# Optimization experiments

Hardware: AMD Instinct MI355X
Metric: run time of the kernel (lower is better)

The kernel has to match this reference:

```python
import jax, jax.numpy as jnp
import numpy as np

B, S, D = 64, 8192, 64

def setup_inputs() -> dict:
    key = jax.random.key(0)
    kq, kk, kv = jax.random.split(key, 3)
    q = jax.random.normal(kq, (B, S, D), dtype=jnp.float32)
    k = jax.random.normal(kk, (B, S, D), dtype=jnp.float32)
    v = jax.random.normal(kv, (B, S, D), dtype=jnp.float32)
    return {"q": q, "k": k, "v": v}

def _feature_map(x):
    # ELU(x) + 1
    return jax.nn.elu(x) + 1.0

def reference(q, k, v):
    qf = _feature_map(q)              # [B, S, D]
    kf = _feature_map(k)              # [B, S, D]
    k_sum = kf.sum(axis=-2)           # [B, D]
    kv = jnp.einsum('bsd,bse->bde', kf, v)        # [B, D, D]
    deno = jnp.maximum(jnp.einsum('bsd,bd->bs', qf, k_sum), 1e-4)  # [B, S]
    o = jnp.einsum('bsd,bde->bse', qf, kv) / deno[..., None]       # [B, S, D]
    return o
```

## Files before the change

kernel.cpp:

```cpp
#include <hip/hip_runtime.h>
#include <math.h>

#define BB 64
#define SS 8192
#define DD 64

constexpr int C1 = 8;
constexpr int CHUNK1 = SS / C1;
constexpr int TROWS  = 128;
constexpr int TILES1 = CHUNK1 / TROWS;

typedef __attribute__((ext_vector_type(8))) short bf16x8;
typedef __attribute__((ext_vector_type(4))) float f32x4;

__device__ __forceinline__ float fmap(float x) {
    return x > 0.0f ? x + 1.0f : __expf(x);
}

__device__ __forceinline__ short f2bf(float x) {
    unsigned int u = __float_as_uint(x);
    u += 0x7FFFu + ((u >> 16) & 1u);
    return (short)(u >> 16);
}

__device__ __forceinline__ void split8(const float* x, bf16x8& hi, bf16x8& lo) {
    #pragma unroll
    for (int i = 0; i < 8; ++i) {
        unsigned int u = __float_as_uint(x[i]);
        hi[i] = (short)(u >> 16);
        float l = x[i] - __uint_as_float(u & 0xFFFF0000u);
        lo[i] = f2bf(l);
    }
}

__device__ __forceinline__ void gload_lds16(const float* gsrc, float* ldst) {
    __builtin_amdgcn_global_load_lds(
        (const __attribute__((address_space(1))) unsigned int*)gsrc,
        (__attribute__((address_space(3))) unsigned int*)ldst,
        16, 0, 0);
}

__global__ __launch_bounds__(256) void phase1_kernel(
    const float* __restrict__ k,
    const float* __restrict__ v,
    float* __restrict__ kvT_ws,
    float* __restrict__ ksum_ws)
{
    __shared__ float Ks[2][TROWS * 64];
    __shared__ float Vs[2][TROWS * 64];

    const int t    = threadIdx.x;
    const int lane = t & 63;
    const int w    = t >> 6;
    const int g    = lane >> 4;
    const int c    = lane & 15;
    const int b    = blockIdx.y;

    const size_t base = (size_t)b * SS * DD + (size_t)blockIdx.x * CHUNK1 * DD;
    const float* kb = k + base;
    const float* vb = v + base;

    auto issue_tile = [&](int tt, int buf) {
        const float* kt = kb + tt * (TROWS * 64);
        const float* vt = vb + tt * (TROWS * 64);
        #pragma unroll
        for (int i = 0; i < 8; ++i) {
            const int Lidx = (w * 8 + i) * 64 + lane;
            const int s    = Lidx >> 4;
            const int p    = Lidx & 15;
            const int gch  = p ^ (((s >> 3) & 1) << 2);
            const int goff = s * 64 + gch * 4;
            const int loff = (w * 8 + i) * 256;
            gload_lds16(kt + goff, &Ks[buf][loff]);
            gload_lds16(vt + goff, &Vs[buf][loff]);
        }
    };

    f32x4 acc[4][4] = {};
    float ksa[4] = {};

    issue_tile(0, 0);
    __syncthreads();

    for (int tt = 0; tt < TILES1; ++tt) {
        const int cur = tt & 1;
        if (tt + 1 < TILES1) issue_tile(tt + 1, cur ^ 1);

        const float* Kc = Ks[cur];
        const float* Vc = Vs[cur];
        const int srow = w * 32 + g * 8;
        const int sw   = (g & 1) << 2;

        bf16x8 Ah[4], Al[4];
        #pragma unroll
        for (int et = 0; et < 4; ++et) {
            const int dc   = et * 16 + c;
            const int bidx = srow * 64 + ((((dc >> 2) ^ sw)) << 2) + (dc & 3);
            float x[8];
            #pragma unroll
            for (int i = 0; i < 8; ++i) x[i] = Vc[bidx + i * 64];
            split8(x, Ah[et], Al[et]);
        }
        #pragma unroll
        for (int dt = 0; dt < 4; ++dt) {
            const int dc   = dt * 16 + c;
            const int bidx = srow * 64 + ((((dc >> 2) ^ sw)) << 2) + (dc & 3);
            float y[8];
            #pragma unroll
            for (int i = 0; i < 8; ++i) y[i] = fmap(Kc[bidx + i * 64]);
            ksa[dt] += ((y[0] + y[1]) + (y[2] + y[3])) + ((y[4] + y[5]) + (y[6] + y[7]));
            bf16x8 Bh, Bl;
            split8(y, Bh, Bl);
            #pragma unroll
            for (int et = 0; et < 4; ++et) {
                acc[et][dt] = __builtin_amdgcn_mfma_f32_16x16x32_bf16(Ah[et], Bh, acc[et][dt], 0, 0, 0);
                acc[et][dt] = __builtin_amdgcn_mfma_f32_16x16x32_bf16(Ah[et], Bl, acc[et][dt], 0, 0, 0);
                acc[et][dt] = __builtin_amdgcn_mfma_f32_16x16x32_bf16(Al[et], Bh, acc[et][dt], 0, 0, 0);
            }
        }
        __syncthreads();
    }

    #pragma unroll
    for (int dt = 0; dt < 4; ++dt) {
        float s = ksa[dt];
        s += __shfl_xor(s, 16, 64);
        s += __shfl_xor(s, 32, 64);
        ksa[dt] = s;
    }
    if (lane < 16) {
        #pragma unroll
        for (int dt = 0; dt < 4; ++dt)
            atomicAdd(ksum_ws + b * DD + dt * 16 + lane, ksa[dt]);
    }

    float* scr = &Ks[0][0] + w * 4096;
    #pragma unroll
    for (int et = 0; et < 4; ++et)
        #pragma unroll
        for (int dt = 0; dt < 4; ++dt)
            #pragma unroll
            for (int r = 0; r < 4; ++r) {
                const int e = et * 16 + 4 * g + r;
                const int d = dt * 16 + c;
                scr[e * 64 + d] = acc[et][dt][r];
            }
    __syncthreads();
    float* kvb = kvT_ws + (size_t)b * DD * DD;
    const float* s0 = &Ks[0][0];
    #pragma unroll
    for (int jj = 0; jj < 16; ++jj) {
        const int i = jj * 256 + t;
        const float vsum = (s0[i] + s0[4096 + i]) + (s0[8192 + i] + s0[12288 + i]);
        atomicAdd(kvb + i, vsum);
    }
}

__global__ __launch_bounds__(256) void phase2_kernel(
    const float* __restrict__ q,
    const float* __restrict__ kvT_ws,
    const float* __restrict__ ksum_ws,
    float* __restrict__ o)
{
    const int t    = threadIdx.x;
    const int lane = t & 63;
    const int w    = t >> 6;
    const int b    = blockIdx.y;
    const int wid  = blockIdx.x * 4 + w;
    const int g    = lane >> 4;
    const int c    = lane & 15;

    const float* kvb = kvT_ws + (size_t)b * DD * DD;
    bf16x8 Bfrag[4][2];
    #pragma unroll
    for (int et = 0; et < 4; ++et) {
        #pragma unroll
        for (int dk = 0; dk < 2; ++dk) {
            const float* p = kvb + (et * 16 + c) * DD + dk * 32 + g * 8;
            float4 lo = *(const float4*)p;
            float4 hi = *(const float4*)(p + 4);
            bf16x8 f;
            f[0] = f2bf(lo.x); f[1] = f2bf(lo.y); f[2] = f2bf(lo.z); f[3] = f2bf(lo.w);
            f[4] = f2bf(hi.x); f[5] = f2bf(hi.y); f[6] = f2bf(hi.z); f[7] = f2bf(hi.w);
            Bfrag[et][dk] = f;
        }
    }
    float ksr[16];
    #pragma unroll
    for (int dk = 0; dk < 2; ++dk) {
        const float* p = ksum_ws + b * DD + dk * 32 + g * 8;
        float4 lo = *(const float4*)p;
        float4 hi = *(const float4*)(p + 4);
        ksr[dk*8+0] = lo.x; ksr[dk*8+1] = lo.y; ksr[dk*8+2] = lo.z; ksr[dk*8+3] = lo.w;
        ksr[dk*8+4] = hi.x; ksr[dk*8+5] = hi.y; ksr[dk*8+6] = hi.z; ksr[dk*8+7] = hi.w;
    }

    const float* qb = q + (size_t)b * SS * DD;
    float*       ob = o + (size_t)b * SS * DD;

    #pragma unroll 1
    for (int tt = 0; tt < 8; ++tt) {
        const int s0 = wid * 128 + tt * 16;
        const float* qrow = qb + (size_t)(s0 + c) * DD;
        float qf[16];
        #pragma unroll
        for (int dk = 0; dk < 2; ++dk) {
            float4 lo = *(const float4*)(qrow + dk * 32 + g * 8);
            float4 hi = *(const float4*)(qrow + dk * 32 + g * 8 + 4);
            qf[dk*8+0] = fmap(lo.x); qf[dk*8+1] = fmap(lo.y);
            qf[dk*8+2] = fmap(lo.z); qf[dk*8+3] = fmap(lo.w);
            qf[dk*8+4] = fmap(hi.x); qf[dk*8+5] = fmap(hi.y);
            qf[dk*8+6] = fmap(hi.z); qf[dk*8+7] = fmap(hi.w);
        }
        float dn = 0.0f;
        #pragma unroll
        for (int i = 0; i < 16; ++i) dn += qf[i] * ksr[i];
        dn += __shfl_xor(dn, 16, 64);
        dn += __shfl_xor(dn, 32, 64);

        bf16x8 A0, A1;
        #pragma unroll
        for (int i = 0; i < 8; ++i) { A0[i] = f2bf(qf[i]); A1[i] = f2bf(qf[8+i]); }

        f32x4 acc0 = {0.f,0.f,0.f,0.f}, acc1 = {0.f,0.f,0.f,0.f};
        f32x4 acc2 = {0.f,0.f,0.f,0.f}, acc3 = {0.f,0.f,0.f,0.f};
        acc0 = __builtin_amdgcn_mfma_f32_16x16x32_bf16(A0, Bfrag[0][0], acc0, 0, 0, 0);
        acc0 = __builtin_amdgcn_mfma_f32_16x16x32_bf16(A1, Bfrag[0][1], acc0, 0, 0, 0);
        acc1 = __builtin_amdgcn_mfma_f32_16x16x32_bf16(A0, Bfrag[1][0], acc1, 0, 0, 0);
        acc1 = __builtin_amdgcn_mfma_f32_16x16x32_bf16(A1, Bfrag[1][1], acc1, 0, 0, 0);
        acc2 = __builtin_amdgcn_mfma_f32_16x16x32_bf16(A0, Bfrag[2][0], acc2, 0, 0, 0);
        acc2 = __builtin_amdgcn_mfma_f32_16x16x32_bf16(A1, Bfrag[2][1], acc2, 0, 0, 0);
        acc3 = __builtin_amdgcn_mfma_f32_16x16x32_bf16(A0, Bfrag[3][0], acc3, 0, 0, 0);
        acc3 = __builtin_amdgcn_mfma_f32_16x16x32_bf16(A1, Bfrag[3][1], acc3, 0, 0, 0);

        #pragma unroll
        for (int r = 0; r < 4; ++r) {
            float dr  = __shfl(dn, (g << 2) + r, 64);
            float inv = 1.0f / fmaxf(dr, 1e-4f);
            float* op = ob + (size_t)(s0 + (g << 2) + r) * DD + c;
            op[0]  = acc0[r] * inv;
            op[16] = acc1[r] * inv;
            op[32] = acc2[r] * inv;
            op[48] = acc3[r] * inv;
        }
    }
}

extern "C" void kernel_launch(void* const* d_in, const int* in_sizes, int n_in,
                              void* d_out, int out_size, void* d_ws, size_t ws_size,
                              hipStream_t stream) {
    const float* q = (const float*)d_in[0];
    const float* k = (const float*)d_in[1];
    const float* v = (const float*)d_in[2];
    float* o = (float*)d_out;

    float* kvT_ws  = (float*)d_ws;
    float* ksum_ws = kvT_ws + (size_t)BB * DD * DD;
    const size_t ws_bytes = ((size_t)BB * DD * DD + (size_t)BB * DD) * sizeof(float);

    hipMemsetAsync(d_ws, 0, ws_bytes, stream);

    dim3 g1(C1, BB), g2(16, BB), blk(256);
    phase1_kernel<<<g1, blk, 0, stream>>>(k, v, kvT_ws, ksum_ws);
    phase2_kernel<<<g2, blk, 0, stream>>>(q, kvT_ws, ksum_ws, o);
}
```

Baseline: 416.3 us.

## Split phase1 KV outer product across warps by d-half and add q prefetch

Phase 1 tile rows are halved to 64. The four warps now split work as two row-halves times two d-halves, so each warp holds a 4x2 accumulator grid instead of 4x4. The cross-warp reduction changes to pairwise summing through shared memory before the global atomics. Fewer accumulator registers and a smaller LDS footprint should allow higher occupancy, at the cost of reloading the V fragments in each warp of a pair. Phase 2 prefetches the next q tile into registers to overlap global loads with compute.

```diff
diff --git a/kernel.cpp b/kernel.cpp
--- a/kernel.cpp
+++ b/kernel.cpp
@@ -7,7 +7,7 @@
 
 constexpr int C1 = 8;
 constexpr int CHUNK1 = SS / C1;
-constexpr int TROWS  = 128;
+constexpr int TROWS  = 64;
 constexpr int TILES1 = CHUNK1 / TROWS;
 
 typedef __attribute__((ext_vector_type(8))) short bf16x8;
@@ -55,6 +55,8 @@
     const int g    = lane >> 4;
     const int c    = lane & 15;
     const int b    = blockIdx.y;
+    const int step = w & 1;
+    const int dh   = w >> 1;
 
     const size_t base = (size_t)b * SS * DD + (size_t)blockIdx.x * CHUNK1 * DD;
     const float* kb = k + base;
@@ -64,20 +66,20 @@
         const float* kt = kb + tt * (TROWS * 64);
         const float* vt = vb + tt * (TROWS * 64);
         #pragma unroll
-        for (int i = 0; i < 8; ++i) {
-            const int Lidx = (w * 8 + i) * 64 + lane;
+        for (int i = 0; i < 4; ++i) {
+            const int Lidx = i * 256 + t;
             const int s    = Lidx >> 4;
             const int p    = Lidx & 15;
             const int gch  = p ^ (((s >> 3) & 1) << 2);
             const int goff = s * 64 + gch * 4;
-            const int loff = (w * 8 + i) * 256;
+            const int loff = (i * 256 + w * 64) * 4;
             gload_lds16(kt + goff, &Ks[buf][loff]);
             gload_lds16(vt + goff, &Vs[buf][loff]);
         }
     };
 
-    f32x4 acc[4][4] = {};
-    float ksa[4] = {};
+    f32x4 acc[4][2] = {};
+    float ksa[2] = {};
 
     issue_tile(0, 0);
     __syncthreads();
@@ -88,71 +90,87 @@
 
         const float* Kc = Ks[cur];
         const float* Vc = Vs[cur];
-        const int srow = w * 32 + g * 8;
+        const int srow = step * 32 + g * 8;
         const int sw   = (g & 1) << 2;
 
         bf16x8 Ah[4], Al[4];
         #pragma unroll
         for (int et = 0; et < 4; ++et) {
             const int dc   = et * 16 + c;
-            const int bidx = srow * 64 + ((((dc >> 2) ^ sw)) << 2) + (dc & 3);
+            const int bidx = srow * 64 + (((dc >> 2) ^ sw) << 2) + (dc & 3);
             float x[8];
             #pragma unroll
             for (int i = 0; i < 8; ++i) x[i] = Vc[bidx + i * 64];
             split8(x, Ah[et], Al[et]);
         }
         #pragma unroll
-        for (int dt = 0; dt < 4; ++dt) {
-            const int dc   = dt * 16 + c;
-            const int bidx = srow * 64 + ((((dc >> 2) ^ sw)) << 2) + (dc & 3);
+        for (int j = 0; j < 2; ++j) {
+            const int dc   = (dh * 2 + j) * 16 + c;
+            const int bidx = srow * 64 + (((dc >> 2) ^ sw) << 2) + (dc & 3);
             float y[8];
             #pragma unroll
             for (int i = 0; i < 8; ++i) y[i] = fmap(Kc[bidx + i * 64]);
-            ksa[dt] += ((y[0] + y[1]) + (y[2] + y[3])) + ((y[4] + y[5]) + (y[6] + y[7]));
+            ksa[j] += ((y[0] + y[1]) + (y[2] + y[3])) + ((y[4] + y[5]) + (y[6] + y[7]));
             bf16x8 Bh, Bl;
             split8(y, Bh, Bl);
             #pragma unroll
             for (int et = 0; et < 4; ++et) {
-                acc[et][dt] = __builtin_amdgcn_mfma_f32_16x16x32_bf16(Ah[et], Bh, acc[et][dt], 0, 0, 0);
-                acc[et][dt] = __builtin_amdgcn_mfma_f32_16x16x32_bf16(Ah[et], Bl, acc[et][dt], 0, 0, 0);
-                acc[et][dt] = __builtin_amdgcn_mfma_f32_16x16x32_bf16(Al[et], Bh, acc[et][dt], 0, 0, 0);
+                acc[et][j] = __builtin_amdgcn_mfma_f32_16x16x32_bf16(Ah[et], Bh, acc[et][j], 0, 0, 0);
+                acc[et][j] = __builtin_amdgcn_mfma_f32_16x16x32_bf16(Ah[et], Bl, acc[et][j], 0, 0, 0);
+                acc[et][j] = __builtin_amdgcn_mfma_f32_16x16x32_bf16(Al[et], Bh, acc[et][j], 0, 0, 0);
             }
         }
         __syncthreads();
     }
 
     #pragma unroll
-    for (int dt = 0; dt < 4; ++dt) {
-        float s = ksa[dt];
+    for (int j = 0; j < 2; ++j) {
+        float s = ksa[j];
         s += __shfl_xor(s, 16, 64);
         s += __shfl_xor(s, 32, 64);
-        ksa[dt] = s;
+        ksa[j] = s;
     }
     if (lane < 16) {
         #pragma unroll
-        for (int dt = 0; dt < 4; ++dt)
-            atomicAdd(ksum_ws + b * DD + dt * 16 + lane, ksa[dt]);
-    }
-
-    float* scr = &Ks[0][0] + w * 4096;
-    #pragma unroll
-    for (int et = 0; et < 4; ++et)
-        #pragma unroll
-        for (int dt = 0; dt < 4; ++dt)
-            #pragma unroll
-            for (int r = 0; r < 4; ++r) {
-                const int e = et * 16 + 4 * g + r;
-                const int d = dt * 16 + c;
-                scr[e * 64 + d] = acc[et][dt][r];
-            }
+        for (int j = 0; j < 2; ++j)
+            atomicAdd(ksum_ws + b * DD + (dh * 2 + j) * 16 + lane, ksa[j]);
+    }
+
+    {
+        float* scr = &Ks[0][0] + dh * 2048;
+        if (step == 1) {
+            #pragma unroll
+            for (int et = 0; et < 4; ++et)
+                #pragma unroll
+                for (int j = 0; j < 2; ++j)
+                    #pragma unroll
+                    for (int r = 0; r < 4; ++r)
+                        scr[((et * 2 + j) * 4 + r) * 64 + lane] = acc[et][j][r];
+        }
+    }
+    __syncthreads();
+    if (step == 0) {
+        const float* scr = &Ks[0][0] + dh * 2048;
+        float* cscr = &Vs[0][0];
+        #pragma unroll
+        for (int et = 0; et < 4; ++et)
+            #pragma unroll
+            for (int j = 0; j < 2; ++j)
+                #pragma unroll
+                for (int r = 0; r < 4; ++r) {
+                    const float s = acc[et][j][r] + scr[((et * 2 + j) * 4 + r) * 64 + lane];
+                    const int e = et * 16 + 4 * g + r;
+                    const int d = (dh * 2 + j) * 16 + c;
+                    cscr[e * 64 + d] = s;
+                }
+    }
     __syncthreads();
     float* kvb = kvT_ws + (size_t)b * DD * DD;
-    const float* s0 = &Ks[0][0];
+    const float* cscr = &Vs[0][0];
     #pragma unroll
     for (int jj = 0; jj < 16; ++jj) {
         const int i = jj * 256 + t;
-        const float vsum = (s0[i] + s0[4096 + i]) + (s0[8192 + i] + s0[12288 + i]);
-        atomicAdd(kvb + i, vsum);
+        atomicAdd(kvb + i, cscr[i]);
     }
 }
 
@@ -198,20 +216,29 @@
     const float* qb = q + (size_t)b * SS * DD;
     float*       ob = o + (size_t)b * SS * DD;
 
+    const float* qrow = qb + (size_t)(wid * 128 + c) * DD;
+    float4 p0 = *(const float4*)(qrow + g * 8);
+    float4 p1 = *(const float4*)(qrow + g * 8 + 4);
+    float4 p2 = *(const float4*)(qrow + 32 + g * 8);
+    float4 p3 = *(const float4*)(qrow + 32 + g * 8 + 4);
+
     #pragma unroll 1
     for (int tt = 0; tt < 8; ++tt) {
         const int s0 = wid * 128 + tt * 16;
-        const float* qrow = qb + (size_t)(s0 + c) * DD;
+        float4 c0 = p0, c1 = p1, c2 = p2, c3 = p3;
+        if (tt < 7) {
+            const float* qn = qb + (size_t)(s0 + 16 + c) * DD;
+            p0 = *(const float4*)(qn + g * 8);
+            p1 = *(const float4*)(qn + g * 8 + 4);
+            p2 = *(const float4*)(qn + 32 + g * 8);
+            p3 = *(const float4*)(qn + 32 + g * 8 + 4);
+        }
         float qf[16];
-        #pragma unroll
-        for (int dk = 0; dk < 2; ++dk) {
-            float4 lo = *(const float4*)(qrow + dk * 32 + g * 8);
-            float4 hi = *(const float4*)(qrow + dk * 32 + g * 8 + 4);
-            qf[dk*8+0] = fmap(lo.x); qf[dk*8+1] = fmap(lo.y);
-            qf[dk*8+2] = fmap(lo.z); qf[dk*8+3] = fmap(lo.w);
-            qf[dk*8+4] = fmap(hi.x); qf[dk*8+5] = fmap(hi.y);
-            qf[dk*8+6] = fmap(hi.z); qf[dk*8+7] = fmap(hi.w);
-        }
+        qf[0]  = fmap(c0.x); qf[1]  = fmap(c0.y); qf[2]  = fmap(c0.z); qf[3]  = fmap(c0.w);
+        qf[4]  = fmap(c1.x); qf[5]  = fmap(c1.y); qf[6]  = fmap(c1.z); qf[7]  = fmap(c1.w);
+        qf[8]  = fmap(c2.x); qf[9]  = fmap(c2.y); qf[10] = fmap(c2.z); qf[11] = fmap(c2.w);
+        qf[12] = fmap(c3.x); qf[13] = fmap(c3.y); qf[14] = fmap(c3.z); qf[15] = fmap(c3.w);
+
         float dn = 0.0f;
         #pragma unroll
         for (int i = 0; i < 16; ++i) dn += qf[i] * ksr[i];
```

Measured after the change: 407.7 us. 2.0% less time.
